# Kernel optimization log

Hardware: AMD Instinct MI355X
Metric: run time of the kernel (lower is better)

Reference implementation:

```python
import jax, jax.numpy as jnp
import numpy as np
import math

B, H, L = 8, 512, 2048
CH = 1          # channels
D2 = 32         # d_state // 2 (conjugate pairs)
DT_MIN, DT_MAX = 0.001, 0.1


def setup_inputs() -> dict:
    key = jax.random.key(0)
    ks = jax.random.split(key, 7)
    u = jax.random.normal(ks[0], (B, H, L), dtype=jnp.float32)
    # Chebyshev initialization (SimpleS4)
    h_scale = jnp.exp(jnp.arange(H, dtype=jnp.float32) / H * math.log(DT_MAX / DT_MIN))
    angles = jnp.arange(D2, dtype=jnp.float32) * jnp.pi
    theta = jnp.broadcast_to(angles[None, None, :], (CH, H, D2)).astype(jnp.float32) + 0.0
    a = -(jnp.broadcast_to(h_scale[None, :, None], (CH, H, D2)).astype(jnp.float32) + 0.0)
    b = jax.random.normal(ks[1], (CH, H, D2), dtype=jnp.float32)
    c = jax.random.normal(ks[2], (CH, H, D2), dtype=jnp.float32)
    x0 = jax.random.normal(ks[3], (CH, H, D2), dtype=jnp.float32)
    D = jax.random.normal(ks[4], (CH, H), dtype=jnp.float32)
    lim = 1.0 / math.sqrt(CH * H)
    W = jax.random.uniform(ks[5], (H, CH * H), minval=-lim, maxval=lim, dtype=jnp.float32)
    bias = jax.random.uniform(ks[6], (H,), minval=-lim, maxval=lim, dtype=jnp.float32)
    return dict(u=u, a=a, theta=theta, b=b, c=c, x0=x0, D=D, W=W, bias=bias)


def fft_conv(u, f):
    # u: (B,H,L), f: (C,H,L) -> causal conv (B,C,H,L) via zero-padded FFT
    n = 2 * u.shape[-1]
    u_f = jnp.fft.rfft(u, n=n)
    f_f = jnp.fft.rfft(f, n=n)
    y = jnp.fft.irfft(jnp.einsum('bhl,chl->bchl', u_f, f_f), n=n)
    return y[..., : u.shape[-1]]


def s4_forward(u, a, theta, b, c, x0, D, W, bias):
    Bsz, Hd, l = u.shape
    T = 1.0 / (l - 1)                                   # quadrature step
    z = T * jnp.arange(l, dtype=u.dtype)                # (L,)
    aa = -jnp.abs(a)                                    # (C,H,D2) stable decay
    # Vandermonde-like basis: exp(a z) cos(theta z), shape (C,H,D2,L)
    base = jnp.exp(aa[..., None] * z) * jnp.cos(theta[..., None] * z)
    q = b * c                                           # (C,H,D2)
    f = 2.0 * T * jnp.einsum('chd,chdl->chl', q, base)  # SSM kernel (C,H,L)
    y = fft_conv(u, f)                                  # (B,C,H,L)
    # trapezoid-rule endpoint correction
    y = y - 0.5 * (jnp.einsum('ch,bhl->bchl', f[:, :, 0], u)
                   + jnp.einsum('chl,bh->bchl', f, u[:, :, 0]))
    # initial-state contribution (x0 term)
    k0 = 2.0 * jnp.einsum('chd,chdl->chl', c * x0, base)
    y = y + k0[None]
    # skip connection D*u
    y = y + jnp.einsum('ch,bhl->bchl', D, u)
    y = y.reshape(Bsz, CH * Hd, l)                      # (B, C*H, L)
    # NonLinear head: GELU -> pointwise Linear(C*H -> H) (transposed conv1x1)
    y = jax.nn.gelu(y, approximate=False)
    out = jnp.einsum('hf,bfl->bhl', W, y) + bias[None, :, None]
    return out


def reference(u, a, theta, b, c, x0, D, W, bias):
    return s4_forward(u, a, theta, b, c, x0, D, W, bias)
```

## Files before the change

kernel.cpp:

```cpp
#include <hip/hip_runtime.h>
#include <hip/hip_bf16.h>

#define B_  8
#define H_  512
#define L_  2048
#define D2_ 32
#define NC_ 64
#define LC_ 32
#define LCF 32
#define EP  36

typedef __attribute__((ext_vector_type(8))) short short8;
typedef __attribute__((ext_vector_type(4))) float float4v;
typedef __attribute__((ext_vector_type(2))) float f32x2;

__device__ __forceinline__ f32x2 pk_fma(f32x2 a, f32x2 b, f32x2 c) {
    return __builtin_elementwise_fma(a, b, c);
}

__device__ __forceinline__ float gelu_exact(float x) {
    return 0.5f * x * (1.0f + erff(x * 0.70710678118654752f));
}

__device__ __forceinline__ unsigned pack_bf16x2(float x, float y) {
    __hip_bfloat162 p = __float22bfloat162_rn(make_float2(x, y));
    return *(unsigned*)&p;
}
__device__ __forceinline__ float2 unpack_bf16x2(unsigned v) {
    __hip_bfloat162 p = *(__hip_bfloat162*)&v;
    return __bfloat1622float2(p);
}

__device__ __forceinline__ void load_lds16(const void* g, void* l) {
    __builtin_amdgcn_global_load_lds((const __attribute__((address_space(1))) unsigned int*)g,
                                     (__attribute__((address_space(3))) unsigned int*)l, 16, 0, 0);
}

__global__ void cast_prep_kernel(const float* __restrict__ W, __hip_bfloat16* __restrict__ Wb,
                                 const float* __restrict__ a, const float* __restrict__ th,
                                 const float* __restrict__ bb, const float* __restrict__ cc,
                                 const float* __restrict__ x0,
                                 float* __restrict__ aT, float* __restrict__ thT,
                                 float* __restrict__ qT, float* __restrict__ gxT,
                                 float* __restrict__ WPp) {
    int tid = blockIdx.x * 256 + threadIdx.x;
    Wb[tid] = __float2bfloat16(W[tid]);
    if (tid < H_ * D2_) {
        int h = tid & (H_ - 1);
        int d = tid >> 9;
        const float T = 1.0f / (float)(L_ - 1);
        float av = -fabsf(a[h * D2_ + d]);
        float tv = th[h * D2_ + d];
        float q  = bb[h * D2_ + d] * cc[h * D2_ + d];
        aT[tid]  = av;
        thT[tid] = tv;
        qT[tid]  = q;
        gxT[tid] = 2.0f * cc[h * D2_ + d] * x0[h * D2_ + d];
        #pragma unroll
        for (int k = 0; k < 6; ++k) {
            float len = (float)(32 << k);
            float e2  = __expf(av * T * len);
            float an  = tv * T * len;
            WPp[((size_t)h * 6 + k) * 64 + d]      = e2 * __cosf(an);
            WPp[((size_t)h * 6 + k) * 64 + 32 + d] = e2 * __sinf(an);
        }
    }
}

__global__ __launch_bounds__(256) void fk_kernel(
        const float* __restrict__ aT, const float* __restrict__ thT,
        const float* __restrict__ qT, const float* __restrict__ gxT,
        unsigned* __restrict__ FKf) {
    int t = threadIdx.x;
    int q4 = t & 3, hl = t >> 2;
    int h  = blockIdx.y * 64 + hl;
    int l0 = blockIdx.x * LCF;
    const float T = 1.0f / (float)(L_ - 1);
    float z0 = T * (float)l0;
    float pr[8], pi[8], wr[8], wi[8], qd[8], gx[8];
    #pragma unroll
    for (int j = 0; j < 8; ++j) {
        int idx = (q4 * 8 + j) * H_ + h;
        float aa = aT[idx], tv = thT[idx];
        float e0 = __expf(aa * z0);
        pr[j] = e0 * __cosf(tv * z0);
        pi[j] = e0 * __sinf(tv * z0);
        float e1 = __expf(aa * T);
        wr[j] = e1 * __cosf(tv * T);
        wi[j] = e1 * __sinf(tv * T);
        qd[j] = qT[idx];
        gx[j] = gxT[idx];
    }
    for (int i = 0; i < LCF; ++i) {
        float fa = 0.f, ka = 0.f;
        #pragma unroll
        for (int j = 0; j < 8; ++j) {
            fa = fmaf(qd[j], pr[j], fa);
            ka = fmaf(gx[j], pr[j], ka);
            float nr = fmaf(pr[j], wr[j], -(pi[j] * wi[j]));
            float ni = fmaf(pr[j], wi[j],  (pi[j] * wr[j]));
            pr[j] = nr; pi[j] = ni;
        }
        fa += __shfl_xor(fa, 1); fa += __shfl_xor(fa, 2);
        ka += __shfl_xor(ka, 1); ka += __shfl_xor(ka, 2);
        if (q4 == 0)
            FKf[(size_t)h * L_ + l0 + i] = pack_bf16x2(2.0f * T * fa, ka);
    }
}

__global__ __launch_bounds__(256) void prep2_kernel(
        const float* __restrict__ aT, const float* __restrict__ thT,
        const float* __restrict__ qT, const unsigned* __restrict__ FKf,
        __hip_bfloat16* __restrict__ AB, __hip_bfloat16* __restrict__ CB) {
    int h = blockIdx.x;
    int t = threadIdx.x;
    const float T = 1.0f / (float)(L_ - 1);
    for (int e = t; e < 64 * 32; e += 256) {
        int m = e >> 5, i = e & 31;
        int d = m & 31;
        float av = aT[d * H_ + h], tv = thT[d * H_ + h];
        float z  = T * (float)(31 - i);
        float ex = __expf(av * z);
        float v  = (m < 32) ? ex * __cosf(tv * z) : ex * __sinf(tv * z);
        AB[(size_t)h * 2048 + e] = __float2bfloat16(v);
    }
    unsigned short* CBs = (unsigned short*)CB;
    for (int e = t; e < 32 * 96; e += 256) {
        int i = e / 96, k = e - i * 96;
        if (k < 32) {
            unsigned short bits = 0;
            if (k <= i) bits = (unsigned short)(FKf[(size_t)h * L_ + (i - k)] & 0xFFFFu);
            CBs[(size_t)h * 3072 + e] = bits;
        } else {
            int d = (k < 64) ? k - 32 : k - 64;
            float av = aT[d * H_ + h], tv = thT[d * H_ + h];
            float qs = 2.0f * T * qT[d * H_ + h];
            float z  = T * (float)(i + 1);
            float ex = __expf(av * z);
            float v  = (k < 64) ? qs * ex * __cosf(tv * z) : -qs * ex * __sinf(tv * z);
            CB[(size_t)h * 3072 + e] = __float2bfloat16(v);
        }
    }
}

__global__ __launch_bounds__(128) void scan_mfma_kernel(
        const float* __restrict__ u, const __hip_bfloat16* __restrict__ AB,
        const __hip_bfloat16* __restrict__ CB, const float* __restrict__ WPp,
        const float* __restrict__ Dp, const unsigned* __restrict__ FKf,
        __hip_bfloat16* __restrict__ y) {
    __shared__ unsigned E_lds[2][64 * EP];
    int wid = threadIdx.x >> 6, lane = threadIdx.x & 63;
    int h = blockIdx.x * 2 + wid, b = blockIdx.y;
    int ln = lane & 15, qq = lane >> 4;
    unsigned* El = E_lds[wid];
    const float* ug = u + (size_t)(b * H_ + h) * L_;

    short8 uf[4];
    #pragma unroll
    for (int nb = 0; nb < 4; ++nb) {
        const float* p = ug + (nb * 16 + ln) * 32 + qq * 8;
        float4 a0 = *(const float4*)p;
        float4 a1 = *(const float4*)(p + 4);
        short8 v;
        ((unsigned*)&v)[0] = pack_bf16x2(a0.x, a0.y);
        ((unsigned*)&v)[1] = pack_bf16x2(a0.z, a0.w);
        ((unsigned*)&v)[2] = pack_bf16x2(a1.x, a1.y);
        ((unsigned*)&v)[3] = pack_bf16x2(a1.z, a1.w);
        uf[nb] = v;
    }

    const short* ABh = (const short*)AB + (size_t)h * 64 * 32;
    #pragma unroll
    for (int e = 0; e < 2; ++e) {
        short8 af[2];
        #pragma unroll
        for (int mb = 0; mb < 2; ++mb)
            af[mb] = *(const short8*)&ABh[(e * 32 + mb * 16 + ln) * 32 + qq * 8];
        float4v acc[2][4];
        #pragma unroll
        for (int mb = 0; mb < 2; ++mb)
            #pragma unroll
            for (int nb = 0; nb < 4; ++nb)
                acc[mb][nb] = (float4v){0.f, 0.f, 0.f, 0.f};
        #pragma unroll
        for (int mb = 0; mb < 2; ++mb)
            #pragma unroll
            for (int nb = 0; nb < 4; ++nb)
                acc[mb][nb] = __builtin_amdgcn_mfma_f32_16x16x32_bf16(
                    af[mb], uf[nb], acc[mb][nb], 0, 0, 0);
        #pragma unroll
        for (int mb = 0; mb < 2; ++mb)
            #pragma unroll
            for (int nb = 0; nb < 4; ++nb) {
                int m2 = e * 16 + mb * 8 + qq * 2;
                unsigned p0 = pack_bf16x2(acc[mb][nb][0], acc[mb][nb][1]);
                unsigned p1 = pack_bf16x2(acc[mb][nb][2], acc[mb][nb][3]);
                *(uint2*)&El[(nb * 16 + ln) * EP + m2] = make_uint2(p0, p1);
            }
    }
    __syncthreads();

    int c = lane;
    f32x2 sr2[16], si2[16];
    #pragma unroll
    for (int jj = 0; jj < 4; ++jj) {
        uint4 er = *(const uint4*)&El[c * EP + jj * 4];
        uint4 ei = *(const uint4*)&El[c * EP + 16 + jj * 4];
        unsigned ers[4] = {er.x, er.y, er.z, er.w};
        unsigned eis[4] = {ei.x, ei.y, ei.z, ei.w};
        #pragma unroll
        for (int w = 0; w < 4; ++w) {
            float2 pr = unpack_bf16x2(ers[w]);
            float2 pi = unpack_bf16x2(eis[w]);
            sr2[jj * 4 + w] = (f32x2){pr.x, pr.y};
            si2[jj * 4 + w] = (f32x2){pi.x, pi.y};
        }
    }
    #pragma unroll
    for (int st = 0; st < 6; ++st) {
        int off = 1 << st;
        const float2* mp = (const float2*)(WPp + ((size_t)h * 6 + st) * 64);
        int src  = (c - off) & 63;
        bool act = c >= off;
        #pragma unroll
        for (int j = 0; j < 16; ++j) {
            float pr0 = __shfl(sr2[j].x, src), pr1 = __shfl(sr2[j].y, src);
            float pi0 = __shfl(si2[j].x, src), pi1 = __shfl(si2[j].y, src);
            if (!act) { pr0 = 0.f; pr1 = 0.f; pi0 = 0.f; pi1 = 0.f; }
            f32x2 pr = (f32x2){pr0, pr1};
            f32x2 pi = (f32x2){pi0, pi1};
            float2 mrv = mp[j];
            float2 miv = mp[16 + j];
            f32x2 Mr = (f32x2){mrv.x, mrv.y};
            f32x2 Mi = (f32x2){miv.x, miv.y};
            sr2[j] = pk_fma(pr, Mr, pk_fma(-pi, Mi, sr2[j]));
            si2[j] = pk_fma(pr, Mi, pk_fma( pi, Mr, si2[j]));
        }
    }
    {
        int srcm1 = (c - 1) & 63;
        #pragma unroll
        for (int j = 0; j < 16; ++j) {
            float a0 = __shfl(sr2[j].x, srcm1), a1 = __shfl(sr2[j].y, srcm1);
            float b0 = __shfl(si2[j].x, srcm1), b1 = __shfl(si2[j].y, srcm1);
            if (c == 0) { a0 = 0.f; a1 = 0.f; b0 = 0.f; b1 = 0.f; }
            sr2[j] = (f32x2){a0, a1};
            si2[j] = (f32x2){b0, b1};
        }
    }
    #pragma unroll
    for (int jj = 0; jj < 4; ++jj) {
        uint4 pr, pi;
        pr.x = pack_bf16x2(sr2[jj*4+0].x, sr2[jj*4+0].y);
        pr.y = pack_bf16x2(sr2[jj*4+1].x, sr2[jj*4+1].y);
        pr.z = pack_bf16x2(sr2[jj*4+2].x, sr2[jj*4+2].y);
        pr.w = pack_bf16x2(sr2[jj*4+3].x, sr2[jj*4+3].y);
        pi.x = pack_bf16x2(si2[jj*4+0].x, si2[jj*4+0].y);
        pi.y = pack_bf16x2(si2[jj*4+1].x, si2[jj*4+1].y);
        pi.z = pack_bf16x2(si2[jj*4+2].x, si2[jj*4+2].y);
        pi.w = pack_bf16x2(si2[jj*4+3].x, si2[jj*4+3].y);
        *(uint4*)&El[c * EP + jj * 4] = pr;
        *(uint4*)&El[c * EP + 16 + jj * 4] = pi;
    }
    __syncthreads();

    const short* CBh = (const short*)CB + (size_t)h * 32 * 96;
    float4v acc2[2][4];
    #pragma unroll
    for (int mb = 0; mb < 2; ++mb)
        #pragma unroll
        for (int nb = 0; nb < 4; ++nb)
            acc2[mb][nb] = (float4v){0.f, 0.f, 0.f, 0.f};
    #pragma unroll
    for (int ks = 0; ks < 3; ++ks) {
        short8 a2[2];
        #pragma unroll
        for (int mb = 0; mb < 2; ++mb)
            a2[mb] = *(const short8*)&CBh[(mb * 16 + ln) * 96 + ks * 32 + qq * 8];
        short8 bf_[4];
        if (ks == 0) {
            #pragma unroll
            for (int nb = 0; nb < 4; ++nb) bf_[nb] = uf[nb];
        } else {
            int off = (ks == 1) ? 0 : 16;
            #pragma unroll
            for (int nb = 0; nb < 4; ++nb)
                bf_[nb] = *(const short8*)&El[(nb * 16 + ln) * EP + off + qq * 4];
        }
        #pragma unroll
        for (int mb = 0; mb < 2; ++mb)
            #pragma unroll
            for (int nb = 0; nb < 4; ++nb)
                acc2[mb][nb] = __builtin_amdgcn_mfma_f32_16x16x32_bf16(
                    a2[mb], bf_[nb], acc2[mb][nb], 0, 0, 0);
    }

    float f0; { float2 t0 = unpack_bf16x2(FKf[(size_t)h * L_]); f0 = t0.x; }
    float c0v = Dp[h] - 0.5f * f0;
    float u0  = ug[0];
    float c1v = -0.5f * u0;
    #pragma unroll
    for (int mb = 0; mb < 2; ++mb)
        #pragma unroll
        for (int nb = 0; nb < 4; ++nb) {
            int l0 = (nb * 16 + ln) * 32 + mb * 16 + qq * 4;
            float4 u4 = *(const float4*)(ug + l0);
            uint4 fkv = *(const uint4*)(FKf + (size_t)h * L_ + l0);
            float us[4] = {u4.x, u4.y, u4.z, u4.w};
            unsigned fs[4] = {fkv.x, fkv.y, fkv.z, fkv.w};
            float g[4];
            #pragma unroll
            for (int r = 0; r < 4; ++r) {
                float2 fk = unpack_bf16x2(fs[r]);
                float yv = acc2[mb][nb][r] + fmaf(c0v, us[r], fmaf(c1v, fk.x, fk.y));
                g[r] = gelu_exact(yv);
            }
            uint2 yo;
            yo.x = pack_bf16x2(g[0], g[1]);
            yo.y = pack_bf16x2(g[2], g[3]);
            *(uint2*)((short*)y + (size_t)(b * H_ + h) * L_ + l0) = yo;
        }
}

__global__ __launch_bounds__(256) void transpose_y_kernel(
        const __hip_bfloat16* __restrict__ y, __hip_bfloat16* __restrict__ yT) {
    __shared__ short tile[64][72];
    int l0 = blockIdx.x * 64, f0 = blockIdx.y * 64, b = blockIdx.z;
    int t = threadIdx.x;
    int row = t >> 3, col8 = (t & 7) * 8;
    const short* yg = (const short*)y + (size_t)b * H_ * L_;
    #pragma unroll
    for (int r2 = 0; r2 < 64; r2 += 32)
        *(uint4*)&tile[row + r2][col8] =
            *(const uint4*)&yg[(size_t)(f0 + row + r2) * L_ + l0 + col8];
    __syncthreads();
    short* og = (short*)yT + (size_t)b * L_ * H_;
    #pragma unroll
    for (int r2 = 0; r2 < 64; r2 += 32) {
        int lrow = row + r2;
        short v[8];
        #pragma unroll
        for (int j = 0; j < 8; ++j) v[j] = tile[col8 + j][lrow];
        *(uint4*)&og[(size_t)(l0 + lrow) * H_ + f0 + col8] = *(uint4*)v;
    }
}

__global__ __launch_bounds__(256) void gemm_kernel(
        const __hip_bfloat16* __restrict__ Wb, const __hip_bfloat16* __restrict__ yT,
        const float* __restrict__ bias, float* __restrict__ out) {
    __shared__ __align__(16) short As[128 * 32];
    __shared__ __align__(16) short Bs[128 * 32];
    int l0 = blockIdx.x * 128;
    int h0 = blockIdx.y * 128;
    int b  = blockIdx.z;
    int t    = threadIdx.x;
    int lane = t & 63, wave = t >> 6;
    int m_off = (wave >> 1) * 64, n_off = (wave & 1) * 64;
    int quad = lane >> 4, ln = lane & 15;

    float4v acc[4][4];
    #pragma unroll
    for (int mt = 0; mt < 4; ++mt)
        #pragma unroll
        for (int nt = 0; nt < 4; ++nt)
            acc[mt][nt] = (float4v){0.f, 0.f, 0.f, 0.f};

    const short* Wg = (const short*)Wb;
    const short* Yg = (const short*)(yT + (size_t)b * L_ * H_);

    int r  = t >> 2;
    int qd = t & 3;

    for (int kt = 0; kt < 16; ++kt) {
        int k0 = kt * 32;
        load_lds16(Wg + (h0 + r)      * 512 + k0 + qd * 8, &As[t * 8]);
        load_lds16(Wg + (h0 + r + 64) * 512 + k0 + qd * 8, &As[(t + 256) * 8]);
        load_lds16(Yg + (size_t)(l0 + r)      * 512 + k0 + qd * 8, &Bs[t * 8]);
        load_lds16(Yg + (size_t)(l0 + r + 64) * 512 + k0 + qd * 8, &Bs[(t + 256) * 8]);
        __syncthreads();

        short8 af[4], bf[4];
        #pragma unroll
        for (int mt = 0; mt < 4; ++mt)
            af[mt] = *(const short8*)&As[(m_off + mt * 16 + ln) * 32 + quad * 8];
        #pragma unroll
        for (int nt = 0; nt < 4; ++nt)
            bf[nt] = *(const short8*)&Bs[(n_off + nt * 16 + ln) * 32 + quad * 8];
        #pragma unroll
        for (int mt = 0; mt < 4; ++mt)
            #pragma unroll
            for (int nt = 0; nt < 4; ++nt)
                acc[mt][nt] = __builtin_amdgcn_mfma_f32_16x16x32_bf16(
                    af[mt], bf[nt], acc[mt][nt], 0, 0, 0);
        __syncthreads();
    }

    #pragma unroll
    for (int mt = 0; mt < 4; ++mt) {
        #pragma unroll
        for (int nt = 0; nt < 4; ++nt) {
            int hh = h0 + m_off + mt * 16 + quad * 4;
            int ll = l0 + n_off + nt * 16 + ln;
            #pragma unroll
            for (int r2 = 0; r2 < 4; ++r2)
                out[((size_t)(b * H_ + hh + r2)) * L_ + ll] = acc[mt][nt][r2] + bias[hh + r2];
        }
    }
}

extern "C" void kernel_launch(void* const* d_in, const int* in_sizes, int n_in,
                              void* d_out, int out_size, void* d_ws, size_t ws_size,
                              hipStream_t stream) {
    const float* u    = (const float*)d_in[0];
    const float* a    = (const float*)d_in[1];
    const float* th   = (const float*)d_in[2];
    const float* bb   = (const float*)d_in[3];
    const float* cc   = (const float*)d_in[4];
    const float* x0   = (const float*)d_in[5];
    const float* Dp   = (const float*)d_in[6];
    const float* W    = (const float*)d_in[7];
    const float* bias = (const float*)d_in[8];
    float* out = (float*)d_out;
    char* ws = (char*)d_ws;

    unsigned*       FKf = (unsigned*)ws;
    __hip_bfloat16* yT  = (__hip_bfloat16*)(ws + (4ull  << 20));
    __hip_bfloat16* y   = (__hip_bfloat16*)(ws + (20ull << 20));
    __hip_bfloat16* Wb  = (__hip_bfloat16*)(ws + (36ull << 20));
    __hip_bfloat16* AB  = (__hip_bfloat16*)(ws + (37ull << 20));
    __hip_bfloat16* CB  = (__hip_bfloat16*)(ws + (39ull << 20));
    float* pbase = (float*)(ws + (42ull << 20));
    float *aT  = pbase,           *thT = pbase + 16384, *qT = pbase + 2*16384,
          *gxT = pbase + 3*16384, *WPp = pbase + 4*16384;

    hipLaunchKernelGGL(cast_prep_kernel,  dim3(1024),      dim3(256), 0, stream,
                       W, Wb, a, th, bb, cc, x0, aT, thT, qT, gxT, WPp);
    hipLaunchKernelGGL(fk_kernel,         dim3(L_/LCF, 8), dim3(256), 0, stream,
                       aT, thT, qT, gxT, FKf);
    hipLaunchKernelGGL(prep2_kernel,      dim3(H_),        dim3(256), 0, stream,
                       aT, thT, qT, FKf, AB, CB);
    hipLaunchKernelGGL(scan_mfma_kernel,  dim3(H_/2, B_),  dim3(128), 0, stream,
                       u, AB, CB, WPp, Dp, FKf, y);
    hipLaunchKernelGGL(transpose_y_kernel,dim3(32, 8, 8),  dim3(256), 0, stream, y, yT);
    hipLaunchKernelGGL(gemm_kernel,       dim3(16, 4, 8),  dim3(256), 0, stream,
                       Wb, yT, bias, out);
}
```

Before: 191.8 us.

## Split scan across two waves per head, use fp16 packed math and tanh-style GELU

The scan kernel now assigns one head per block and splits the 32 state pairs and output columns between its two waves, doubling the grid and halving per-wave register and ALU work. The chunk-state scan moves from fp32 packed FMA to fp16 packed FMA, and the MFMA inputs, AB/CB and WP tables switch from bf16 to fp16. FK values for the epilogue are prefetched before the barrier, and exact erf GELU is replaced by a sigmoid-based tanh approximation. This cuts instruction count and raises occupancy, but fp16 state accumulation and approximate GELU add numerical error, and the sched barrier plus manual waitcnt stand in for a block sync.

```diff
diff --git a/kernel.cpp b/kernel.cpp
--- a/kernel.cpp
+++ b/kernel.cpp
@@ -11,15 +11,18 @@
 #define EP  36
 
 typedef __attribute__((ext_vector_type(8))) short short8;
+typedef __attribute__((ext_vector_type(8))) _Float16 half8;
+typedef __attribute__((ext_vector_type(2))) _Float16 half2v;
 typedef __attribute__((ext_vector_type(4))) float float4v;
-typedef __attribute__((ext_vector_type(2))) float f32x2;
-
-__device__ __forceinline__ f32x2 pk_fma(f32x2 a, f32x2 b, f32x2 c) {
+
+__device__ __forceinline__ half2v pk_fma16(half2v a, half2v b, half2v c) {
     return __builtin_elementwise_fma(a, b, c);
 }
 
-__device__ __forceinline__ float gelu_exact(float x) {
-    return 0.5f * x * (1.0f + erff(x * 0.70710678118654752f));
+__device__ __forceinline__ float gelu_fast(float x) {
+    float q = x * fmaf(0.044715f, x * x, 1.0f);
+    float s = __expf(-1.5957691216057308f * q);
+    return __fdividef(x, 1.0f + s);
 }
 
 __device__ __forceinline__ unsigned pack_bf16x2(float x, float y) {
@@ -29,6 +32,10 @@
 __device__ __forceinline__ float2 unpack_bf16x2(unsigned v) {
     __hip_bfloat162 p = *(__hip_bfloat162*)&v;
     return __bfloat1622float2(p);
+}
+__device__ __forceinline__ unsigned pack_f16x2(float x, float y) {
+    auto v = __builtin_amdgcn_cvt_pkrtz(x, y);
+    return *(unsigned*)&v;
 }
 
 __device__ __forceinline__ void load_lds16(const void* g, void* l) {
@@ -42,7 +49,7 @@
                                  const float* __restrict__ x0,
                                  float* __restrict__ aT, float* __restrict__ thT,
                                  float* __restrict__ qT, float* __restrict__ gxT,
-                                 float* __restrict__ WPp) {
+                                 _Float16* __restrict__ WPh) {
     int tid = blockIdx.x * 256 + threadIdx.x;
     Wb[tid] = __float2bfloat16(W[tid]);
     if (tid < H_ * D2_) {
@@ -61,8 +68,8 @@
             float len = (float)(32 << k);
             float e2  = __expf(av * T * len);
             float an  = tv * T * len;
-            WPp[((size_t)h * 6 + k) * 64 + d]      = e2 * __cosf(an);
-            WPp[((size_t)h * 6 + k) * 64 + 32 + d] = e2 * __sinf(an);
+            WPh[((size_t)h * 6 + k) * 64 + d]      = (_Float16)(e2 * __cosf(an));
+            WPh[((size_t)h * 6 + k) * 64 + 32 + d] = (_Float16)(e2 * __sinf(an));
         }
     }
 }
@@ -111,7 +118,7 @@
 __global__ __launch_bounds__(256) void prep2_kernel(
         const float* __restrict__ aT, const float* __restrict__ thT,
         const float* __restrict__ qT, const unsigned* __restrict__ FKf,
-        __hip_bfloat16* __restrict__ AB, __hip_bfloat16* __restrict__ CB) {
+        _Float16* __restrict__ AB, _Float16* __restrict__ CB) {
     int h = blockIdx.x;
     int t = threadIdx.x;
     const float T = 1.0f / (float)(L_ - 1);
@@ -122,204 +129,184 @@
         float z  = T * (float)(31 - i);
         float ex = __expf(av * z);
         float v  = (m < 32) ? ex * __cosf(tv * z) : ex * __sinf(tv * z);
-        AB[(size_t)h * 2048 + e] = __float2bfloat16(v);
-    }
-    unsigned short* CBs = (unsigned short*)CB;
+        AB[(size_t)h * 2048 + e] = (_Float16)v;
+    }
     for (int e = t; e < 32 * 96; e += 256) {
         int i = e / 96, k = e - i * 96;
+        float v = 0.f;
         if (k < 32) {
-            unsigned short bits = 0;
-            if (k <= i) bits = (unsigned short)(FKf[(size_t)h * L_ + (i - k)] & 0xFFFFu);
-            CBs[(size_t)h * 3072 + e] = bits;
+            if (k <= i) {
+                unsigned fw = FKf[(size_t)h * L_ + (i - k)];
+                v = unpack_bf16x2(fw).x;
+            }
         } else {
             int d = (k < 64) ? k - 32 : k - 64;
             float av = aT[d * H_ + h], tv = thT[d * H_ + h];
             float qs = 2.0f * T * qT[d * H_ + h];
             float z  = T * (float)(i + 1);
             float ex = __expf(av * z);
-            float v  = (k < 64) ? qs * ex * __cosf(tv * z) : -qs * ex * __sinf(tv * z);
-            CB[(size_t)h * 3072 + e] = __float2bfloat16(v);
-        }
-    }
-}
-
-__global__ __launch_bounds__(128) void scan_mfma_kernel(
-        const float* __restrict__ u, const __hip_bfloat16* __restrict__ AB,
-        const __hip_bfloat16* __restrict__ CB, const float* __restrict__ WPp,
+            v = (k < 64) ? qs * ex * __cosf(tv * z) : -qs * ex * __sinf(tv * z);
+        }
+        CB[(size_t)h * 3072 + e] = (_Float16)v;
+    }
+}
+
+__global__ __launch_bounds__(128, 6) void scan_mfma_kernel(
+        const float* __restrict__ u, const _Float16* __restrict__ AB,
+        const _Float16* __restrict__ CB, const unsigned* __restrict__ WPh,
         const float* __restrict__ Dp, const unsigned* __restrict__ FKf,
         __hip_bfloat16* __restrict__ y) {
-    __shared__ unsigned E_lds[2][64 * EP];
+    __shared__ __align__(16) unsigned El[64 * EP];
     int wid = threadIdx.x >> 6, lane = threadIdx.x & 63;
-    int h = blockIdx.x * 2 + wid, b = blockIdx.y;
+    int h = blockIdx.x, b = blockIdx.y;
     int ln = lane & 15, qq = lane >> 4;
-    unsigned* El = E_lds[wid];
     const float* ug = u + (size_t)(b * H_ + h) * L_;
 
-    short8 uf[4];
+    half8 uf[4];
     #pragma unroll
     for (int nb = 0; nb < 4; ++nb) {
         const float* p = ug + (nb * 16 + ln) * 32 + qq * 8;
         float4 a0 = *(const float4*)p;
         float4 a1 = *(const float4*)(p + 4);
-        short8 v;
-        ((unsigned*)&v)[0] = pack_bf16x2(a0.x, a0.y);
-        ((unsigned*)&v)[1] = pack_bf16x2(a0.z, a0.w);
-        ((unsigned*)&v)[2] = pack_bf16x2(a1.x, a1.y);
-        ((unsigned*)&v)[3] = pack_bf16x2(a1.z, a1.w);
-        uf[nb] = v;
-    }
-
-    const short* ABh = (const short*)AB + (size_t)h * 64 * 32;
+        unsigned* vp = (unsigned*)&uf[nb];
+        vp[0] = pack_f16x2(a0.x, a0.y);
+        vp[1] = pack_f16x2(a0.z, a0.w);
+        vp[2] = pack_f16x2(a1.x, a1.y);
+        vp[3] = pack_f16x2(a1.z, a1.w);
+    }
+
+    const _Float16* ABh = AB + (size_t)h * 2048;
+    int j0 = wid * 8 + qq * 2;
     #pragma unroll
     for (int e = 0; e < 2; ++e) {
-        short8 af[2];
-        #pragma unroll
-        for (int mb = 0; mb < 2; ++mb)
-            af[mb] = *(const short8*)&ABh[(e * 32 + mb * 16 + ln) * 32 + qq * 8];
-        float4v acc[2][4];
-        #pragma unroll
-        for (int mb = 0; mb < 2; ++mb)
-            #pragma unroll
-            for (int nb = 0; nb < 4; ++nb)
-                acc[mb][nb] = (float4v){0.f, 0.f, 0.f, 0.f};
-        #pragma unroll
-        for (int mb = 0; mb < 2; ++mb)
-            #pragma unroll
-            for (int nb = 0; nb < 4; ++nb)
-                acc[mb][nb] = __builtin_amdgcn_mfma_f32_16x16x32_bf16(
-                    af[mb], uf[nb], acc[mb][nb], 0, 0, 0);
-        #pragma unroll
-        for (int mb = 0; mb < 2; ++mb)
-            #pragma unroll
-            for (int nb = 0; nb < 4; ++nb) {
-                int m2 = e * 16 + mb * 8 + qq * 2;
-                unsigned p0 = pack_bf16x2(acc[mb][nb][0], acc[mb][nb][1]);
-                unsigned p1 = pack_bf16x2(acc[mb][nb][2], acc[mb][nb][3]);
-                *(uint2*)&El[(nb * 16 + ln) * EP + m2] = make_uint2(p0, p1);
-            }
-    }
-    __syncthreads();
+        half8 af = *(const half8*)&ABh[(e * 32 + wid * 16 + ln) * 32 + qq * 8];
+        #pragma unroll
+        for (int nb = 0; nb < 4; ++nb) {
+            float4v acc = (float4v){0.f, 0.f, 0.f, 0.f};
+            acc = __builtin_amdgcn_mfma_f32_16x16x32_f16(af, uf[nb], acc, 0, 0, 0);
+            unsigned p0 = pack_f16x2(acc[0], acc[1]);
+            unsigned p1 = pack_f16x2(acc[2], acc[3]);
+            *(uint2*)&El[(nb * 16 + ln) * EP + e * 16 + j0] = make_uint2(p0, p1);
+        }
+    }
+    asm volatile("s_waitcnt lgkmcnt(0)" ::: "memory");
+    __builtin_amdgcn_sched_barrier(0);
 
     int c = lane;
-    f32x2 sr2[16], si2[16];
-    #pragma unroll
-    for (int jj = 0; jj < 4; ++jj) {
-        uint4 er = *(const uint4*)&El[c * EP + jj * 4];
-        uint4 ei = *(const uint4*)&El[c * EP + 16 + jj * 4];
-        unsigned ers[4] = {er.x, er.y, er.z, er.w};
-        unsigned eis[4] = {ei.x, ei.y, ei.z, ei.w};
-        #pragma unroll
-        for (int w = 0; w < 4; ++w) {
-            float2 pr = unpack_bf16x2(ers[w]);
-            float2 pi = unpack_bf16x2(eis[w]);
-            sr2[jj * 4 + w] = (f32x2){pr.x, pr.y};
-            si2[jj * 4 + w] = (f32x2){pi.x, pi.y};
-        }
-    }
+    unsigned sr[8], si[8];
+    {
+        const unsigned* rp = &El[c * EP + wid * 8];
+        uint4 r0 = *(const uint4*)rp;
+        uint4 r1 = *(const uint4*)(rp + 4);
+        uint4 i0 = *(const uint4*)(rp + 16);
+        uint4 i1 = *(const uint4*)(rp + 20);
+        sr[0]=r0.x; sr[1]=r0.y; sr[2]=r0.z; sr[3]=r0.w;
+        sr[4]=r1.x; sr[5]=r1.y; sr[6]=r1.z; sr[7]=r1.w;
+        si[0]=i0.x; si[1]=i0.y; si[2]=i0.z; si[3]=i0.w;
+        si[4]=i1.x; si[5]=i1.y; si[6]=i1.z; si[7]=i1.w;
+    }
+    const unsigned* mpb = WPh + (size_t)h * 6 * 32;
     #pragma unroll
     for (int st = 0; st < 6; ++st) {
         int off = 1 << st;
-        const float2* mp = (const float2*)(WPp + ((size_t)h * 6 + st) * 64);
-        int src  = (c - off) & 63;
+        int src = (c - off) & 63;
         bool act = c >= off;
-        #pragma unroll
-        for (int j = 0; j < 16; ++j) {
-            float pr0 = __shfl(sr2[j].x, src), pr1 = __shfl(sr2[j].y, src);
-            float pi0 = __shfl(si2[j].x, src), pi1 = __shfl(si2[j].y, src);
-            if (!act) { pr0 = 0.f; pr1 = 0.f; pi0 = 0.f; pi1 = 0.f; }
-            f32x2 pr = (f32x2){pr0, pr1};
-            f32x2 pi = (f32x2){pi0, pi1};
-            float2 mrv = mp[j];
-            float2 miv = mp[16 + j];
-            f32x2 Mr = (f32x2){mrv.x, mrv.y};
-            f32x2 Mi = (f32x2){miv.x, miv.y};
-            sr2[j] = pk_fma(pr, Mr, pk_fma(-pi, Mi, sr2[j]));
-            si2[j] = pk_fma(pr, Mi, pk_fma( pi, Mr, si2[j]));
+        const unsigned* mp = mpb + st * 32 + wid * 8;
+        #pragma unroll
+        for (int jj = 0; jj < 8; ++jj) {
+            unsigned prp = (unsigned)__shfl((int)sr[jj], src);
+            unsigned pip = (unsigned)__shfl((int)si[jj], src);
+            if (!act) { prp = 0u; pip = 0u; }
+            unsigned mru = mp[jj];
+            unsigned miu = mp[16 + jj];
+            unsigned min_ = miu ^ 0x80008000u;
+            half2v pr = *(half2v*)&prp, pi = *(half2v*)&pip;
+            half2v Mr = *(half2v*)&mru, Mi = *(half2v*)&miu, Mni = *(half2v*)&min_;
+            half2v s_r = *(half2v*)&sr[jj], s_i = *(half2v*)&si[jj];
+            half2v nr = pk_fma16(pr, Mr, pk_fma16(pi, Mni, s_r));
+            half2v ni = pk_fma16(pr, Mi, pk_fma16(pi, Mr,  s_i));
+            sr[jj] = *(unsigned*)&nr; si[jj] = *(unsigned*)&ni;
         }
     }
     {
         int srcm1 = (c - 1) & 63;
         #pragma unroll
-        for (int j = 0; j < 16; ++j) {
-            float a0 = __shfl(sr2[j].x, srcm1), a1 = __shfl(sr2[j].y, srcm1);
-            float b0 = __shfl(si2[j].x, srcm1), b1 = __shfl(si2[j].y, srcm1);
-            if (c == 0) { a0 = 0.f; a1 = 0.f; b0 = 0.f; b1 = 0.f; }
-            sr2[j] = (f32x2){a0, a1};
-            si2[j] = (f32x2){b0, b1};
-        }
-    }
-    #pragma unroll
-    for (int jj = 0; jj < 4; ++jj) {
-        uint4 pr, pi;
-        pr.x = pack_bf16x2(sr2[jj*4+0].x, sr2[jj*4+0].y);
-        pr.y = pack_bf16x2(sr2[jj*4+1].x, sr2[jj*4+1].y);
-        pr.z = pack_bf16x2(sr2[jj*4+2].x, sr2[jj*4+2].y);
-        pr.w = pack_bf16x2(sr2[jj*4+3].x, sr2[jj*4+3].y);
-        pi.x = pack_bf16x2(si2[jj*4+0].x, si2[jj*4+0].y);
-        pi.y = pack_bf16x2(si2[jj*4+1].x, si2[jj*4+1].y);
-        pi.z = pack_bf16x2(si2[jj*4+2].x, si2[jj*4+2].y);
-        pi.w = pack_bf16x2(si2[jj*4+3].x, si2[jj*4+3].y);
-        *(uint4*)&El[c * EP + jj * 4] = pr;
-        *(uint4*)&El[c * EP + 16 + jj * 4] = pi;
+        for (int jj = 0; jj < 8; ++jj) {
+            unsigned a0 = (unsigned)__shfl((int)sr[jj], srcm1);
+            unsigned b0 = (unsigned)__shfl((int)si[jj], srcm1);
+            if (c == 0) { a0 = 0u; b0 = 0u; }
+            sr[jj] = a0; si[jj] = b0;
+        }
+    }
+    {
+        unsigned* wp = &El[c * EP + wid * 8];
+        *(uint4*)wp        = make_uint4(sr[0], sr[1], sr[2], sr[3]);
+        *(uint4*)(wp + 4)  = make_uint4(sr[4], sr[5], sr[6], sr[7]);
+        *(uint4*)(wp + 16) = make_uint4(si[0], si[1], si[2], si[3]);
+        *(uint4*)(wp + 20) = make_uint4(si[4], si[5], si[6], si[7]);
+    }
+    const unsigned* fgh = FKf + (size_t)h * L_;
+    uint4 fkp[2][2];
+    #pragma unroll
+    for (int nbi = 0; nbi < 2; ++nbi) {
+        int col = (2 * wid + nbi) * 16 + ln;
+        fkp[nbi][0] = *(const uint4*)&fgh[col * 32 + qq * 4];
+        fkp[nbi][1] = *(const uint4*)&fgh[col * 32 + 16 + qq * 4];
     }
     __syncthreads();
 
-    const short* CBh = (const short*)CB + (size_t)h * 32 * 96;
-    float4v acc2[2][4];
+    const _Float16* CBh = CB + (size_t)h * 3072;
+    float4v acc2[2][2];
     #pragma unroll
     for (int mb = 0; mb < 2; ++mb)
         #pragma unroll
-        for (int nb = 0; nb < 4; ++nb)
-            acc2[mb][nb] = (float4v){0.f, 0.f, 0.f, 0.f};
+        for (int nbi = 0; nbi < 2; ++nbi)
+            acc2[mb][nbi] = (float4v){0.f, 0.f, 0.f, 0.f};
     #pragma unroll
     for (int ks = 0; ks < 3; ++ks) {
-        short8 a2[2];
-        #pragma unroll
-        for (int mb = 0; mb < 2; ++mb)
-            a2[mb] = *(const short8*)&CBh[(mb * 16 + ln) * 96 + ks * 32 + qq * 8];
-        short8 bf_[4];
-        if (ks == 0) {
-            #pragma unroll
-            for (int nb = 0; nb < 4; ++nb) bf_[nb] = uf[nb];
-        } else {
-            int off = (ks == 1) ? 0 : 16;
-            #pragma unroll
-            for (int nb = 0; nb < 4; ++nb)
-                bf_[nb] = *(const short8*)&El[(nb * 16 + ln) * EP + off + qq * 4];
-        }
-        #pragma unroll
-        for (int mb = 0; mb < 2; ++mb)
-            #pragma unroll
-            for (int nb = 0; nb < 4; ++nb)
-                acc2[mb][nb] = __builtin_amdgcn_mfma_f32_16x16x32_bf16(
-                    a2[mb], bf_[nb], acc2[mb][nb], 0, 0, 0);
-    }
-
-    float f0; { float2 t0 = unpack_bf16x2(FKf[(size_t)h * L_]); f0 = t0.x; }
+        half8 a2[2];
+        a2[0] = *(const half8*)&CBh[(ln)      * 96 + ks * 32 + qq * 8];
+        a2[1] = *(const half8*)&CBh[(16 + ln) * 96 + ks * 32 + qq * 8];
+        #pragma unroll
+        for (int nbi = 0; nbi < 2; ++nbi) {
+            int col = (2 * wid + nbi) * 16 + ln;
+            half8 bfv;
+            if (ks == 0) bfv = uf[2 * wid + nbi];
+            else {
+                int off = (ks == 1) ? 0 : 16;
+                bfv = *(const half8*)&El[col * EP + off + qq * 4];
+            }
+            acc2[0][nbi] = __builtin_amdgcn_mfma_f32_16x16x32_f16(a2[0], bfv, acc2[0][nbi], 0, 0, 0);
+            acc2[1][nbi] = __builtin_amdgcn_mfma_f32_16x16x32_f16(a2[1], bfv, acc2[1][nbi], 0, 0, 0);
+        }
+    }
+
+    float f0; { f0 = unpack_bf16x2(fgh[0]).x; }
     float c0v = Dp[h] - 0.5f * f0;
-    float u0  = ug[0];
-    float c1v = -0.5f * u0;
-    #pragma unroll
-    for (int mb = 0; mb < 2; ++mb)
-        #pragma unroll
-        for (int nb = 0; nb < 4; ++nb) {
-            int l0 = (nb * 16 + ln) * 32 + mb * 16 + qq * 4;
+    float c1v = -0.5f * ug[0];
+    #pragma unroll
+    for (int nbi = 0; nbi < 2; ++nbi) {
+        int col = (2 * wid + nbi) * 16 + ln;
+        #pragma unroll
+        for (int mb = 0; mb < 2; ++mb) {
+            int l0 = col * 32 + mb * 16 + qq * 4;
             float4 u4 = *(const float4*)(ug + l0);
-            uint4 fkv = *(const uint4*)(FKf + (size_t)h * L_ + l0);
+            uint4 fkv = fkp[nbi][mb];
             float us[4] = {u4.x, u4.y, u4.z, u4.w};
             unsigned fs[4] = {fkv.x, fkv.y, fkv.z, fkv.w};
             float g[4];
             #pragma unroll
             for (int r = 0; r < 4; ++r) {
                 float2 fk = unpack_bf16x2(fs[r]);
-                float yv = acc2[mb][nb][r] + fmaf(c0v, us[r], fmaf(c1v, fk.x, fk.y));
-                g[r] = gelu_exact(yv);
+                float yv = acc2[mb][nbi][r] + fmaf(c0v, us[r], fmaf(c1v, fk.x, fk.y));
+                g[r] = gelu_fast(yv);
             }
             uint2 yo;
             yo.x = pack_bf16x2(g[0], g[1]);
             yo.y = pack_bf16x2(g[2], g[3]);
             *(uint2*)((short*)y + (size_t)(b * H_ + h) * L_ + l0) = yo;
         }
+    }
 }
 
 __global__ __launch_bounds__(256) void transpose_y_kernel(
@@ -427,20 +414,21 @@
     __hip_bfloat16* yT  = (__hip_bfloat16*)(ws + (4ull  << 20));
     __hip_bfloat16* y   = (__hip_bfloat16*)(ws + (20ull << 20));
     __hip_bfloat16* Wb  = (__hip_bfloat16*)(ws + (36ull << 20));
-    __hip_bfloat16* AB  = (__hip_bfloat16*)(ws + (37ull << 20));
-    __hip_bfloat16* CB  = (__hip_bfloat16*)(ws + (39ull << 20));
+    _Float16*       AB  = (_Float16*)(ws + (37ull << 20));
+    _Float16*       CB  = (_Float16*)(ws + (39ull << 20));
     float* pbase = (float*)(ws + (42ull << 20));
     float *aT  = pbase,           *thT = pbase + 16384, *qT = pbase + 2*16384,
-          *gxT = pbase + 3*16384, *WPp = pbase + 4*16384;
+          *gxT = pbase + 3*16384;
+    _Float16* WPh = (_Float16*)(pbase + 4*16384);
 
     hipLaunchKernelGGL(cast_prep_kernel,  dim3(1024),      dim3(256), 0, stream,
-                       W, Wb, a, th, bb, cc, x0, aT, thT, qT, gxT, WPp);
+                       W, Wb, a, th, bb, cc, x0, aT, thT, qT, gxT, WPh);
     hipLaunchKernelGGL(fk_kernel,         dim3(L_/LCF, 8), dim3(256), 0, stream,
                        aT, thT, qT, gxT, FKf);
     hipLaunchKernelGGL(prep2_kernel,      dim3(H_),        dim3(256), 0, stream,
                        aT, thT, qT, FKf, AB, CB);
-    hipLaunchKernelGGL(scan_mfma_kernel,  dim3(H_/2, B_),  dim3(128), 0, stream,
-                       u, AB, CB, WPp, Dp, FKf, y);
+    hipLaunchKernelGGL(scan_mfma_kernel,  dim3(H_, B_),    dim3(128), 0, stream,
+                       u, AB, CB, (const unsigned*)WPh, Dp, FKf, y);
     hipLaunchKernelGGL(transpose_y_kernel,dim3(32, 8, 8),  dim3(256), 0, stream, y, yT);
     hipLaunchKernelGGL(gemm_kernel,       dim3(16, 4, 8),  dim3(256), 0, stream,
                        Wb, yT, bias, out);
```

Result: faster. 177.8 us (-7.3%).
